# Optimization experiments

Measured on AMD Instinct MI355X. Metric: run time of the kernel, lower is better.

## Reference

```python
import jax, jax.numpy as jnp
import numpy as np

EMBED = 256
HEADS = 8
LEVELS = 4
POINTS = 4
HD = EMBED // HEADS  # 32
SHAPES = [(100, 100), (50, 50), (25, 25), (13, 13)]  # (H, W) per level
NV = sum(h * w for h, w in SHAPES)  # 13294
BS = 2


def _lin_params(k, fan_in, fan_out):
    s = 1.0 / np.sqrt(fan_in)
    kw, kb = jax.random.split(k)
    W = jax.random.uniform(kw, (fan_in, fan_out), jnp.float32, -s, s)
    b = jax.random.uniform(kb, (fan_out,), jnp.float32, -s, s)
    return W, b


def setup_inputs():
    key = jax.random.key(0)
    ks = jax.random.split(key, 10)
    inp = {
        "query": jax.random.normal(ks[0], (BS, NV, EMBED), jnp.float32),
        "key": jax.random.normal(ks[1], (BS, NV, EMBED), jnp.float32),
        "value": jax.random.normal(ks[2], (BS, NV, EMBED), jnp.float32),
        "query_pos": jax.random.normal(ks[3], (BS, NV, EMBED), jnp.float32),
        "reference_points": jax.random.uniform(ks[4], (BS, NV, LEVELS, 2), jnp.float32),
        "spatial_shapes": jnp.array(SHAPES, jnp.int32),
        "level_start_index": jnp.array(np.cumsum([0] + [h * w for h, w in SHAPES[:-1]]), jnp.int32),
        "key_padding_mask": jnp.zeros((BS, NV), bool),
    }
    inp["W_value"], inp["b_value"] = _lin_params(ks[5], EMBED, EMBED)
    inp["W_off"], inp["b_off"] = _lin_params(ks[6], EMBED, HEADS * LEVELS * POINTS * 2)
    inp["W_attn"], inp["b_attn"] = _lin_params(ks[7], EMBED, HEADS * LEVELS * POINTS)
    inp["W_out"], inp["b_out"] = _lin_params(ks[8], EMBED, EMBED)
    inp["W_ffn"], inp["b_ffn"] = _lin_params(ks[9], EMBED, EMBED)
    return inp


def _bilinear(v, x, y, H, W):
    # v: (bs, heads, H*W, hd); x, y: (bs, heads, n) pixel coords (align_corners=False)
    # zero padding outside the feature map (matches torch grid_sample padding_mode='zeros')
    x0 = jnp.floor(x)
    y0 = jnp.floor(y)
    lx = x - x0
    ly = y - y0
    x0 = x0.astype(jnp.int32)
    y0 = y0.astype(jnp.int32)

    def g(xi, yi):
        valid = ((xi >= 0) & (xi < W) & (yi >= 0) & (yi < H)).astype(v.dtype)
        idx = jnp.clip(yi, 0, H - 1) * W + jnp.clip(xi, 0, W - 1)
        return jnp.take_along_axis(v, idx[..., None], axis=2) * valid[..., None]

    return (g(x0, y0) * ((1 - lx) * (1 - ly))[..., None]
            + g(x0 + 1, y0) * (lx * (1 - ly))[..., None]
            + g(x0, y0 + 1) * ((1 - lx) * ly)[..., None]
            + g(x0 + 1, y0 + 1) * (lx * ly)[..., None])


def _forward(query, key, value, query_pos, reference_points, shapes, starts,
             key_padding_mask, W_value, b_value, W_off, b_off, W_attn, b_attn,
             W_out, b_out, W_ffn, b_ffn):
    bs, nq, _ = query.shape
    identity = query  # residual taken BEFORE adding positional encoding (mmcv semantics)
    q = query + query_pos
    v = value @ W_value + b_value
    v = jnp.where(key_padding_mask[..., None], 0.0, v).reshape(bs, -1, HEADS, HD)
    off = (q @ W_off + b_off).reshape(bs, nq, HEADS, LEVELS, POINTS, 2)
    aw = jax.nn.softmax((q @ W_attn + b_attn).reshape(bs, nq, HEADS, LEVELS * POINTS), axis=-1)
    aw = aw.reshape(bs, nq, HEADS, LEVELS, POINTS)
    # offset normalizer is (W, H) per level
    wh = jnp.array([[w, h] for h, w in shapes], jnp.float32)
    loc = reference_points[:, :, None, :, None, :] + off / wh[None, None, None, :, None, :]
    out = jnp.zeros((bs, HEADS, nq, HD), q.dtype)
    for l, (H, W) in enumerate(shapes):
        s = starts[l]
        vl = v[:, s:s + H * W].transpose(0, 2, 1, 3)  # (bs, heads, H*W, hd)
        x = (loc[:, :, :, l, :, 0] * W - 0.5).transpose(0, 2, 1, 3).reshape(bs, HEADS, nq * POINTS)
        y = (loc[:, :, :, l, :, 1] * H - 0.5).transpose(0, 2, 1, 3).reshape(bs, HEADS, nq * POINTS)
        smp = _bilinear(vl, x, y, H, W).reshape(bs, HEADS, nq, POINTS, HD)
        wl = aw[:, :, :, l].transpose(0, 2, 1, 3)  # (bs, heads, nq, P)
        out = out + jnp.sum(smp * wl[..., None], axis=3)
    out = out.transpose(0, 2, 1, 3).reshape(bs, nq, EMBED)
    out = out @ W_out + b_out + identity
    return out @ W_ffn + b_ffn


def reference(query, key, value, query_pos, reference_points, spatial_shapes,
              level_start_index, key_padding_mask, W_value, b_value, W_off, b_off,
              W_attn, b_attn, W_out, b_out, W_ffn, b_ffn):
    # spatial shapes / level starts are structural metadata -> treat as static ints
    shapes = [tuple(int(x) for x in r) for r in np.asarray(spatial_shapes)]
    starts = [int(x) for x in np.asarray(level_start_index)]
    return _forward(query, key, value, query_pos, reference_points, shapes, starts,
                    key_padding_mask, W_value, b_value, W_off, b_off, W_attn, b_attn,
                    W_out, b_out, W_ffn, b_ffn)
```

## Files before the change

kernel.cpp:

```cpp
#include <hip/hip_runtime.h>
#include <hip/hip_bf16.h>
#include <math.h>

#define NQ 13294
#define NV 13294
#define M_ROWS (2*NQ)
#define MP 26624

typedef __attribute__((ext_vector_type(8))) short bf16x8;
typedef __attribute__((ext_vector_type(4))) float f32x4;
typedef __attribute__((ext_vector_type(2))) float f32x2;

__device__ __forceinline__ float4 ld4(const float* p){ return *(const float4*)p; }
__device__ __forceinline__ float bfu_lo(unsigned int u){ return __uint_as_float(u << 16); }
__device__ __forceinline__ float bfu_hi(unsigned int u){ return __uint_as_float(u & 0xffff0000u); }
__device__ __forceinline__ f32x2 up2(unsigned int u){
  return (f32x2){__uint_as_float(u << 16), __uint_as_float(u & 0xffff0000u)};
}
__device__ __forceinline__ unsigned short f2bf(float f){
  unsigned int u = __float_as_uint(f);
  u += 0x7fffu + ((u >> 16) & 1u);
  return (unsigned short)(u >> 16);
}
__device__ __forceinline__ unsigned int pk2(float a, float b){
  return (unsigned int)f2bf(a) | ((unsigned int)f2bf(b) << 16);
}
__device__ __forceinline__ void gl_lds16(const unsigned short* g, unsigned short* l) {
  __builtin_amdgcn_global_load_lds(
      (const __attribute__((address_space(1))) unsigned int*)g,
      (__attribute__((address_space(3))) unsigned int*)l, 16, 0, 0);
}

__global__ __launch_bounds__(256) void prep_all(
    const float* __restrict__ value, const float* __restrict__ query,
    const float* __restrict__ qpos,
    unsigned short* __restrict__ val_bf, unsigned short* __restrict__ q_bf,
    const float* __restrict__ wv, const float* __restrict__ wo,
    const float* __restrict__ wa, const float* __restrict__ wu,
    const float* __restrict__ wf, unsigned short* __restrict__ wt)
{
  const int total = MP * 64;
  for (int i = blockIdx.x * 256 + threadIdx.x; i < total; i += gridDim.x * 256) {
    const int e = i * 4;
    ushort4 a = make_ushort4(0,0,0,0), b = make_ushort4(0,0,0,0);
    if (e < M_ROWS * 256) {
      float4 v4 = ld4(value + e);
      a = make_ushort4(f2bf(v4.x), f2bf(v4.y), f2bf(v4.z), f2bf(v4.w));
      float4 q4 = ld4(query + e);
      float4 p4 = ld4(qpos + e);
      b = make_ushort4(f2bf(q4.x+p4.x), f2bf(q4.y+p4.y), f2bf(q4.z+p4.z), f2bf(q4.w+p4.w));
    }
    *(ushort4*)(val_bf + e) = a;
    *(ushort4*)(q_bf   + e) = b;
  }
  for (int t = blockIdx.x * 256 + threadIdx.x; t < 294912; t += gridDim.x * 256) {
    const float* src; int Nn; int base;
    if      (t < 65536)  { src = wv; Nn = 256; base = 0; }
    else if (t < 131072) { src = wo; Nn = 256; base = 65536; }
    else if (t < 163840) { src = wa; Nn = 128; base = 131072; }
    else if (t < 229376) { src = wu; Nn = 256; base = 163840; }
    else                 { src = wf; Nn = 256; base = 229376; }
    const int local = t - base;
    const int n = local >> 8, k = local & 255;
    wt[t] = f2bf(src[k * Nn + n]);
  }
}

template<int NCOL, int OUT_MODE, bool ADD_RES>
__global__ __launch_bounds__(256) void gemm_gl(
    const unsigned short* __restrict__ A, const unsigned short* __restrict__ Bt,
    const float* __restrict__ biasA, const float* __restrict__ biasB,
    const float* __restrict__ RES, void* __restrict__ Cv, int N)
{
  __shared__ unsigned short lds[32768];

  const int nwg = 416 * NCOL;
  const int lin = blockIdx.x;
  const int swz = (lin & 7) * (nwg >> 3) + (lin >> 3);
  const int brow = (swz / NCOL) * 64;
  const int bcol = (swz % NCOL) * 64;

  const int tid  = threadIdx.x;
  const int wid  = tid >> 6, lane = tid & 63;
  const int wr   = wid >> 1, wc = wid & 1;
  const int fr   = lane & 15, fg = lane >> 4;

  {
    const int r0   = lane >> 3;
    const int slot = lane & 7;
    #pragma unroll
    for (int t = 0; t < 4; ++t) {
      #pragma unroll
      for (int c = 0; c < 2; ++c) {
        const int row = (wid * 2 + c) * 8 + r0;
        const int gsl = slot ^ (row & 7);
        gl_lds16(A  + (size_t)(brow + row) * 256 + t * 64 + (gsl << 3),
                 &lds[t * 4096 + (wid * 2 + c) * 512]);
        gl_lds16(Bt + (size_t)(bcol + row) * 256 + t * 64 + (gsl << 3),
                 &lds[16384 + t * 4096 + (wid * 2 + c) * 512]);
      }
    }
  }
  __syncthreads();

  f32x4 acc[2][2];
  #pragma unroll
  for (int m = 0; m < 2; ++m)
    #pragma unroll
    for (int n = 0; n < 2; ++n)
      acc[m][n] = (f32x4){0.f, 0.f, 0.f, 0.f};

  #pragma unroll
  for (int t = 0; t < 4; ++t) {
    const char* as = (const char*)&lds[t * 4096];
    const char* bs = (const char*)&lds[16384 + t * 4096];
    #pragma unroll
    for (int kk = 0; kk < 2; ++kk) {
      const int kb = kk * 64 + fg * 16;
      bf16x8 af[2], bfv[2];
      #pragma unroll
      for (int m = 0; m < 2; ++m) {
        const int r = wr * 32 + m * 16 + fr;
        af[m] = *(const bf16x8*)(as + r * 128 + (kb ^ ((r & 7) << 4)));
      }
      #pragma unroll
      for (int n = 0; n < 2; ++n) {
        const int r = wc * 32 + n * 16 + fr;
        bfv[n] = *(const bf16x8*)(bs + r * 128 + (kb ^ ((r & 7) << 4)));
      }
      #pragma unroll
      for (int m = 0; m < 2; ++m)
        #pragma unroll
        for (int n = 0; n < 2; ++n)
          acc[m][n] = __builtin_amdgcn_mfma_f32_16x16x32_bf16(af[m], bfv[n], acc[m][n], 0, 0, 0);
    }
  }

  __syncthreads();
  float* csh = (float*)lds;
  const int c0 = bcol + wc * 32 + fr;
  const int c1 = c0 + 16;
  const float bn0 = (c0 < 256) ? biasA[c0] : biasB[c0 - 256];
  const float bn1 = (c1 < 256) ? biasA[c1] : biasB[c1 - 256];
  #pragma unroll
  for (int m = 0; m < 2; ++m)
    #pragma unroll
    for (int j = 0; j < 4; ++j) {
      const int row = wr * 32 + m * 16 + fg * 4 + j;
      csh[row * 64 + wc * 32 + fr]      = acc[m][0][j] + bn0;
      csh[row * 64 + wc * 32 + 16 + fr] = acc[m][1][j] + bn1;
    }
  __syncthreads();
  #pragma unroll
  for (int i = 0; i < 4; ++i) {
    const int rl = i * 16 + (tid >> 4);
    const int gr = brow + rl;
    if (gr >= M_ROWS) continue;
    const int c4 = (tid & 15) * 4;
    float4 v = *(const float4*)&csh[rl * 64 + c4];
    if (ADD_RES) {
      float4 q = ld4(RES + (size_t)gr * 256 + bcol + c4);
      v.x += q.x; v.y += q.y; v.z += q.z; v.w += q.w;
    }
    if (OUT_MODE == 0) {
      *(float4*)&((float*)Cv)[(size_t)gr * N + bcol + c4] = v;
    } else if (OUT_MODE == 1) {
      ushort4 pk = make_ushort4(f2bf(v.x), f2bf(v.y), f2bf(v.z), f2bf(v.w));
      *(ushort4*)&((unsigned short*)Cv)[(size_t)gr * N + bcol + c4] = pk;
    } else {
      const int head = (bcol + c4) >> 5;
      const int ch   = c4 & 31;
      ushort4 pk = make_ushort4(f2bf(v.x), f2bf(v.y), f2bf(v.z), f2bf(v.w));
      *(ushort4*)&((unsigned short*)Cv)[((size_t)head * M_ROWS + gr) * 32 + ch] = pk;
    }
  }
}

__global__ __launch_bounds__(256) void msda6(
    const unsigned short* __restrict__ v, const unsigned short* __restrict__ oa,
    const float* __restrict__ ref, unsigned short* __restrict__ attout)
{
  constexpr int LW[4] = {100, 50, 25, 13};
  constexpr int LS[4] = {0, 10000, 12500, 13125};

  __shared__ int2   sidx[32][17];
  __shared__ float4 swt [32][17];

  const int bid   = blockIdx.x;
  const int h     = bid & 7;
  const int chunk = bid >> 3;
  const int tid   = threadIdx.x;
  const int q     = tid >> 3;
  const int c     = tid & 7;
  const int bq    = chunk * 32 + q;
  const bool active = bq < M_ROWS;
  const int b     = (bq >= NQ) ? 1 : 0;

  if (active) {
    const int l = c >> 1;
    const int W = LW[l];
    const float fD = (float)W;
    const unsigned short* oarow = oa + (size_t)bq * 384;

    unsigned int lgu = *(const unsigned int*)(oarow + 256 + h * 16 + c * 2);
    float g0 = bfu_lo(lgu), g1 = bfu_hi(lgu);
    float mx = fmaxf(g0, g1);
    mx = fmaxf(mx, __shfl_xor(mx, 1));
    mx = fmaxf(mx, __shfl_xor(mx, 2));
    mx = fmaxf(mx, __shfl_xor(mx, 4));
    float e0 = __expf(g0 - mx), e1 = __expf(g1 - mx);
    float s = e0 + e1;
    s += __shfl_xor(s, 1);
    s += __shfl_xor(s, 2);
    s += __shfl_xor(s, 4);
    const float inv = 1.f / s;
    const float wpt[2] = {e0 * inv, e1 * inv};

    uint2 ou = *(const uint2*)(oarow + h * 32 + c * 4);
    const float oxy[4] = {bfu_lo(ou.x), bfu_hi(ou.x), bfu_lo(ou.y), bfu_hi(ou.y)};
    const float rx = ref[(size_t)bq * 8 + l * 2];
    const float ry = ref[(size_t)bq * 8 + l * 2 + 1];
    const int rowbase = b * NV + LS[l];

    #pragma unroll
    for (int j = 0; j < 2; ++j) {
      const float x = fmaf(rx, fD, oxy[2*j])   - 0.5f;
      const float y = fmaf(ry, fD, oxy[2*j+1]) - 0.5f;
      const float x0f = floorf(x), y0f = floorf(y);
      const float lx = x - x0f, ly = y - y0f;
      const int x0 = (int)x0f, y0 = (int)y0f;
      const int y1 = y0 + 1;
      const int xbase = min(max(x0, 0), W - 2);
      const float wx0 = 1.f - lx, wx1 = lx;
      const float we0 = (x0 == xbase     ? wx0 : 0.f) + (x0 == xbase - 1 ? wx1 : 0.f);
      const float we1 = (x0 == xbase + 1 ? wx0 : 0.f) + (x0 == xbase     ? wx1 : 0.f);
      const int cy0 = min(max(y0, 0), W - 1), cy1 = min(max(y1, 0), W - 1);
      const float wy0 = (y0 >= 0 && y0 < W) ? (1.f - ly) : 0.f;
      const float wy1 = (y1 >= 0 && y1 < W) ? ly : 0.f;
      const float wt = wpt[j];
      const int p = c * 2 + j;
      sidx[q][p] = make_int2((rowbase + cy0 * W + xbase) * 64,
                             (rowbase + cy1 * W + xbase) * 64);
      swt[q][p] = make_float4(wt * wy0 * we0, wt * wy0 * we1,
                              wt * wy1 * we0, wt * wy1 * we1);
    }
  }
  __syncthreads();

  if (active) {
    const char* vb = (const char*)v + (size_t)h * M_ROWS * 64 + c * 16;
    const int el = c >> 2;
    f32x2 acc2[4];
    #pragma unroll
    for (int k = 0; k < 4; ++k) acc2[k] = (f32x2){0.f, 0.f};
    #pragma unroll
    for (int p = 0; p < 16; ++p) {
      const int2   ix = sidx[q][p];
      const float4 w4 = swt[q][p];
      uint4 r0 = *(const uint4*)(vb + ix.x);
      uint4 r1 = *(const uint4*)(vb + ix.y);
      const float wa = el ? w4.y : w4.x;
      const float wb = el ? w4.w : w4.z;
      const f32x2 wav = (f32x2){wa, wa};
      const f32x2 wbv = (f32x2){wb, wb};
      acc2[0] = wav * up2(r0.x) + acc2[0];
      acc2[1] = wav * up2(r0.y) + acc2[1];
      acc2[2] = wav * up2(r0.z) + acc2[2];
      acc2[3] = wav * up2(r0.w) + acc2[3];
      acc2[0] = wbv * up2(r1.x) + acc2[0];
      acc2[1] = wbv * up2(r1.y) + acc2[1];
      acc2[2] = wbv * up2(r1.z) + acc2[2];
      acc2[3] = wbv * up2(r1.w) + acc2[3];
    }
    #pragma unroll
    for (int k = 0; k < 4; ++k) {
      acc2[k][0] += __shfl_xor(acc2[k][0], 4);
      acc2[k][1] += __shfl_xor(acc2[k][1], 4);
    }
    if (c < 4) {
      uint4 pk;
      pk.x = pk2(acc2[0][0], acc2[0][1]);
      pk.y = pk2(acc2[1][0], acc2[1][1]);
      pk.z = pk2(acc2[2][0], acc2[2][1]);
      pk.w = pk2(acc2[3][0], acc2[3][1]);
      *(uint4*)(attout + (size_t)bq * 256 + h * 32 + c * 8) = pk;
    }
  }
}

extern "C" void kernel_launch(void* const* d_in, const int* in_sizes, int n_in,
                              void* d_out, int out_size, void* d_ws, size_t ws_size,
                              hipStream_t stream) {
  const float* query  = (const float*)d_in[0];
  const float* value  = (const float*)d_in[2];
  const float* qpos   = (const float*)d_in[3];
  const float* refpts = (const float*)d_in[4];
  const float* W_value = (const float*)d_in[8];
  const float* b_value = (const float*)d_in[9];
  const float* W_off   = (const float*)d_in[10];
  const float* b_off   = (const float*)d_in[11];
  const float* W_attn  = (const float*)d_in[12];
  const float* b_attn  = (const float*)d_in[13];
  const float* W_out   = (const float*)d_in[14];
  const float* b_out   = (const float*)d_in[15];
  const float* W_ffn   = (const float*)d_in[16];
  const float* b_ffn   = (const float*)d_in[17];
  float* out = (float*)d_out;

  unsigned short* oa    = (unsigned short*)d_ws;
  unsigned short* vbuf2 = oa + (size_t)MP * 384;
  unsigned short* AB1   = vbuf2 + (size_t)8 * M_ROWS * 32;
  unsigned short* AB2   = AB1 + (size_t)MP * 256;
  unsigned short* wts   = AB2 + (size_t)MP * 256;
  unsigned short* wv_t  = wts;
  unsigned short* woa_t = wts + 65536;
  unsigned short* wu_t  = wts + 163840;
  unsigned short* wf_t  = wts + 229376;

  const dim3 blk(256);

  prep_all<<<dim3(2048), blk, 0, stream>>>(value, query, qpos, AB1, AB2,
      W_value, W_off, W_attn, W_out, W_ffn, wts);

  gemm_gl<4,2,false><<<dim3(1664), blk, 0, stream>>>(
      AB1, wv_t, b_value, b_value, nullptr, vbuf2, 256);
  gemm_gl<6,1,false><<<dim3(2496), blk, 0, stream>>>(
      AB2, woa_t, b_off, b_attn, nullptr, oa, 384);
  msda6<<<dim3(8 * 831), blk, 0, stream>>>(vbuf2, oa, refpts, AB1);
  gemm_gl<4,1,true><<<dim3(1664), blk, 0, stream>>>(
      AB1, wu_t, b_out, b_out, query, AB2, 256);
  gemm_gl<4,0,false><<<dim3(1664), blk, 0, stream>>>(
      AB2, wf_t, b_ffn, b_ffn, nullptr, (void*)out, 256);
}
```

Baseline: 120.9 us.

## Store projected value tensor in FP8 and remap sampling threads to four per query

The value projection epilogue now writes FP8 (packed with cvt_pk_fp8) instead of bf16, halving the bytes gathered by the deformable-attention sampling kernel. The sampling kernel is rewritten so each query uses 4 threads (one per level) instead of 8, each thread handling 4 points and a 16-channel fp8 slice, with 64 queries per block. This cuts gather bandwidth and block count but lowers the precision of sampled values to FP8, which may exceed accuracy tolerances.

```diff
diff --git a/kernel.cpp b/kernel.cpp
--- a/kernel.cpp
+++ b/kernel.cpp
@@ -14,9 +14,6 @@
 __device__ __forceinline__ float4 ld4(const float* p){ return *(const float4*)p; }
 __device__ __forceinline__ float bfu_lo(unsigned int u){ return __uint_as_float(u << 16); }
 __device__ __forceinline__ float bfu_hi(unsigned int u){ return __uint_as_float(u & 0xffff0000u); }
-__device__ __forceinline__ f32x2 up2(unsigned int u){
-  return (f32x2){__uint_as_float(u << 16), __uint_as_float(u & 0xffff0000u)};
-}
 __device__ __forceinline__ unsigned short f2bf(float f){
   unsigned int u = __float_as_uint(f);
   u += 0x7fffu + ((u >> 16) & 1u);
@@ -170,60 +167,61 @@
     } else {
       const int head = (bcol + c4) >> 5;
       const int ch   = c4 & 31;
-      ushort4 pk = make_ushort4(f2bf(v.x), f2bf(v.y), f2bf(v.z), f2bf(v.w));
-      *(ushort4*)&((unsigned short*)Cv)[((size_t)head * M_ROWS + gr) * 32 + ch] = pk;
-    }
-  }
-}
-
-__global__ __launch_bounds__(256) void msda6(
-    const unsigned short* __restrict__ v, const unsigned short* __restrict__ oa,
+      int r = 0;
+      r = __builtin_amdgcn_cvt_pk_fp8_f32(v.x, v.y, r, 0);
+      r = __builtin_amdgcn_cvt_pk_fp8_f32(v.z, v.w, r, 1);
+      *(int*)&((unsigned char*)Cv)[((size_t)head * M_ROWS + gr) * 32 + ch] = r;
+    }
+  }
+}
+
+__global__ __launch_bounds__(256) void msda7(
+    const unsigned char* __restrict__ v, const unsigned short* __restrict__ oa,
     const float* __restrict__ ref, unsigned short* __restrict__ attout)
 {
   constexpr int LW[4] = {100, 50, 25, 13};
   constexpr int LS[4] = {0, 10000, 12500, 13125};
 
-  __shared__ int2   sidx[32][17];
-  __shared__ float4 swt [32][17];
+  __shared__ int2   sidx[64][17];
+  __shared__ float4 swt [64][17];
 
   const int bid   = blockIdx.x;
   const int h     = bid & 7;
   const int chunk = bid >> 3;
   const int tid   = threadIdx.x;
-  const int q     = tid >> 3;
-  const int c     = tid & 7;
-  const int bq    = chunk * 32 + q;
+  const int q     = tid >> 2;
+  const int c     = tid & 3;
+  const int bq    = chunk * 64 + q;
   const bool active = bq < M_ROWS;
   const int b     = (bq >= NQ) ? 1 : 0;
 
   if (active) {
-    const int l = c >> 1;
+    const int l = c;
     const int W = LW[l];
     const float fD = (float)W;
     const unsigned short* oarow = oa + (size_t)bq * 384;
 
-    unsigned int lgu = *(const unsigned int*)(oarow + 256 + h * 16 + c * 2);
-    float g0 = bfu_lo(lgu), g1 = bfu_hi(lgu);
-    float mx = fmaxf(g0, g1);
+    uint2 lg = *(const uint2*)(oarow + 256 + h * 16 + l * 4);
+    float g0 = bfu_lo(lg.x), g1 = bfu_hi(lg.x), g2 = bfu_lo(lg.y), g3 = bfu_hi(lg.y);
+    float mx = fmaxf(fmaxf(g0, g1), fmaxf(g2, g3));
     mx = fmaxf(mx, __shfl_xor(mx, 1));
     mx = fmaxf(mx, __shfl_xor(mx, 2));
-    mx = fmaxf(mx, __shfl_xor(mx, 4));
-    float e0 = __expf(g0 - mx), e1 = __expf(g1 - mx);
-    float s = e0 + e1;
+    float e0 = __expf(g0-mx), e1 = __expf(g1-mx), e2 = __expf(g2-mx), e3 = __expf(g3-mx);
+    float s = e0 + e1 + e2 + e3;
     s += __shfl_xor(s, 1);
     s += __shfl_xor(s, 2);
-    s += __shfl_xor(s, 4);
     const float inv = 1.f / s;
-    const float wpt[2] = {e0 * inv, e1 * inv};
-
-    uint2 ou = *(const uint2*)(oarow + h * 32 + c * 4);
-    const float oxy[4] = {bfu_lo(ou.x), bfu_hi(ou.x), bfu_lo(ou.y), bfu_hi(ou.y)};
+    const float ee[4] = {e0*inv, e1*inv, e2*inv, e3*inv};
+
+    uint4 ov = *(const uint4*)(oarow + h * 32 + l * 8);
+    const float oxy[8] = {bfu_lo(ov.x), bfu_hi(ov.x), bfu_lo(ov.y), bfu_hi(ov.y),
+                          bfu_lo(ov.z), bfu_hi(ov.z), bfu_lo(ov.w), bfu_hi(ov.w)};
     const float rx = ref[(size_t)bq * 8 + l * 2];
     const float ry = ref[(size_t)bq * 8 + l * 2 + 1];
     const int rowbase = b * NV + LS[l];
 
     #pragma unroll
-    for (int j = 0; j < 2; ++j) {
+    for (int j = 0; j < 4; ++j) {
       const float x = fmaf(rx, fD, oxy[2*j])   - 0.5f;
       const float y = fmaf(ry, fD, oxy[2*j+1]) - 0.5f;
       const float x0f = floorf(x), y0f = floorf(y);
@@ -237,10 +235,10 @@
       const int cy0 = min(max(y0, 0), W - 1), cy1 = min(max(y1, 0), W - 1);
       const float wy0 = (y0 >= 0 && y0 < W) ? (1.f - ly) : 0.f;
       const float wy1 = (y1 >= 0 && y1 < W) ? ly : 0.f;
-      const float wt = wpt[j];
-      const int p = c * 2 + j;
-      sidx[q][p] = make_int2((rowbase + cy0 * W + xbase) * 64,
-                             (rowbase + cy1 * W + xbase) * 64);
+      const float wt = ee[j];
+      const int p = l * 4 + j;
+      sidx[q][p] = make_int2((rowbase + cy0 * W + xbase) * 32,
+                             (rowbase + cy1 * W + xbase) * 32);
       swt[q][p] = make_float4(wt * wy0 * we0, wt * wy0 * we1,
                               wt * wy1 * we0, wt * wy1 * we1);
     }
@@ -248,11 +246,11 @@
   __syncthreads();
 
   if (active) {
-    const char* vb = (const char*)v + (size_t)h * M_ROWS * 64 + c * 16;
-    const int el = c >> 2;
-    f32x2 acc2[4];
-    #pragma unroll
-    for (int k = 0; k < 4; ++k) acc2[k] = (f32x2){0.f, 0.f};
+    const unsigned char* vb = v + (size_t)h * M_ROWS * 32 + c * 16;
+    const int el = c >> 1;
+    f32x2 acc2[8];
+    #pragma unroll
+    for (int k = 0; k < 8; ++k) acc2[k] = (f32x2){0.f, 0.f};
     #pragma unroll
     for (int p = 0; p < 16; ++p) {
       const int2   ix = sidx[q][p];
@@ -263,27 +261,41 @@
       const float wb = el ? w4.w : w4.z;
       const f32x2 wav = (f32x2){wa, wa};
       const f32x2 wbv = (f32x2){wb, wb};
-      acc2[0] = wav * up2(r0.x) + acc2[0];
-      acc2[1] = wav * up2(r0.y) + acc2[1];
-      acc2[2] = wav * up2(r0.z) + acc2[2];
-      acc2[3] = wav * up2(r0.w) + acc2[3];
-      acc2[0] = wbv * up2(r1.x) + acc2[0];
-      acc2[1] = wbv * up2(r1.y) + acc2[1];
-      acc2[2] = wbv * up2(r1.z) + acc2[2];
-      acc2[3] = wbv * up2(r1.w) + acc2[3];
-    }
-    #pragma unroll
-    for (int k = 0; k < 4; ++k) {
-      acc2[k][0] += __shfl_xor(acc2[k][0], 4);
-      acc2[k][1] += __shfl_xor(acc2[k][1], 4);
-    }
-    if (c < 4) {
-      uint4 pk;
-      pk.x = pk2(acc2[0][0], acc2[0][1]);
-      pk.y = pk2(acc2[1][0], acc2[1][1]);
-      pk.z = pk2(acc2[2][0], acc2[2][1]);
-      pk.w = pk2(acc2[3][0], acc2[3][1]);
-      *(uint4*)(attout + (size_t)bq * 256 + h * 32 + c * 8) = pk;
+      acc2[0] = wav * __builtin_amdgcn_cvt_pk_f32_fp8(r0.x, 0) + acc2[0];
+      acc2[1] = wav * __builtin_amdgcn_cvt_pk_f32_fp8(r0.x, 1) + acc2[1];
+      acc2[2] = wav * __builtin_amdgcn_cvt_pk_f32_fp8(r0.y, 0) + acc2[2];
+      acc2[3] = wav * __builtin_amdgcn_cvt_pk_f32_fp8(r0.y, 1) + acc2[3];
+      acc2[4] = wav * __builtin_amdgcn_cvt_pk_f32_fp8(r0.z, 0) + acc2[4];
+      acc2[5] = wav * __builtin_amdgcn_cvt_pk_f32_fp8(r0.z, 1) + acc2[5];
+      acc2[6] = wav * __builtin_amdgcn_cvt_pk_f32_fp8(r0.w, 0) + acc2[6];
+      acc2[7] = wav * __builtin_amdgcn_cvt_pk_f32_fp8(r0.w, 1) + acc2[7];
+      acc2[0] = wbv * __builtin_amdgcn_cvt_pk_f32_fp8(r1.x, 0) + acc2[0];
+      acc2[1] = wbv * __builtin_amdgcn_cvt_pk_f32_fp8(r1.x, 1) + acc2[1];
+      acc2[2] = wbv * __builtin_amdgcn_cvt_pk_f32_fp8(r1.y, 0) + acc2[2];
+      acc2[3] = wbv * __builtin_amdgcn_cvt_pk_f32_fp8(r1.y, 1) + acc2[3];
+      acc2[4] = wbv * __builtin_amdgcn_cvt_pk_f32_fp8(r1.z, 0) + acc2[4];
+      acc2[5] = wbv * __builtin_amdgcn_cvt_pk_f32_fp8(r1.z, 1) + acc2[5];
+      acc2[6] = wbv * __builtin_amdgcn_cvt_pk_f32_fp8(r1.w, 0) + acc2[6];
+      acc2[7] = wbv * __builtin_amdgcn_cvt_pk_f32_fp8(r1.w, 1) + acc2[7];
+    }
+    #pragma unroll
+    for (int k = 0; k < 8; ++k) {
+      acc2[k][0] += __shfl_xor(acc2[k][0], 2);
+      acc2[k][1] += __shfl_xor(acc2[k][1], 2);
+    }
+    if (c < 2) {
+      uint4 pkA, pkB;
+      pkA.x = pk2(acc2[0][0], acc2[0][1]);
+      pkA.y = pk2(acc2[1][0], acc2[1][1]);
+      pkA.z = pk2(acc2[2][0], acc2[2][1]);
+      pkA.w = pk2(acc2[3][0], acc2[3][1]);
+      pkB.x = pk2(acc2[4][0], acc2[4][1]);
+      pkB.y = pk2(acc2[5][0], acc2[5][1]);
+      pkB.z = pk2(acc2[6][0], acc2[6][1]);
+      pkB.w = pk2(acc2[7][0], acc2[7][1]);
+      unsigned short* dst = attout + (size_t)bq * 256 + h * 32 + c * 16;
+      *(uint4*)dst = pkA;
+      *(uint4*)(dst + 8) = pkB;
     }
   }
 }
@@ -308,8 +320,8 @@
   float* out = (float*)d_out;
 
   unsigned short* oa    = (unsigned short*)d_ws;
-  unsigned short* vbuf2 = oa + (size_t)MP * 384;
-  unsigned short* AB1   = vbuf2 + (size_t)8 * M_ROWS * 32;
+  unsigned char*  vbuf8 = (unsigned char*)(oa + (size_t)MP * 384);
+  unsigned short* AB1   = (unsigned short*)(vbuf8 + (size_t)8 * M_ROWS * 32);
   unsigned short* AB2   = AB1 + (size_t)MP * 256;
   unsigned short* wts   = AB2 + (size_t)MP * 256;
   unsigned short* wv_t  = wts;
@@ -323,10 +335,10 @@
       W_value, W_off, W_attn, W_out, W_ffn, wts);
 
   gemm_gl<4,2,false><<<dim3(1664), blk, 0, stream>>>(
-      AB1, wv_t, b_value, b_value, nullptr, vbuf2, 256);
+      AB1, wv_t, b_value, b_value, nullptr, vbuf8, 256);
   gemm_gl<6,1,false><<<dim3(2496), blk, 0, stream>>>(
       AB2, woa_t, b_off, b_attn, nullptr, oa, 384);
-  msda6<<<dim3(8 * 831), blk, 0, stream>>>(vbuf2, oa, refpts, AB1);
+  msda7<<<dim3(8 * 416), blk, 0, stream>>>(vbuf8, oa, refpts, AB1);
   gemm_gl<4,1,true><<<dim3(1664), blk, 0, stream>>>(
       AB1, wu_t, b_out, b_out, query, AB2, 256);
   gemm_gl<4,0,false><<<dim3(1664), blk, 0, stream>>>(
```

Measured after the change: 112.7 us. 6.8% less time.
